# Performance work log

Hardware: AMD Instinct MI355X
Metric: run time of the kernel (lower is better)

## Reference

```python
import jax, jax.numpy as jnp
import numpy as np

B, S, D = 4, 2048, 1024
CTX_LEN, CTX_DIM = 77, 768
H, DH = 16, 64
INNER = H * DH
MULT = 4
EPS = 1e-5


def setup_inputs() -> dict:
    key = jax.random.key(0)
    ks = jax.random.split(key, 14)
    nrm = lambda k, shape: jax.random.normal(k, shape, dtype=jnp.float32) * 0.02
    return {
        "x": jax.random.normal(ks[0], (B, S, D), dtype=jnp.float32),
        "context": jax.random.normal(ks[1], (B, CTX_LEN, CTX_DIM), dtype=jnp.float32),
        "ln1_g": jnp.ones((D,), jnp.float32), "ln1_b": jnp.zeros((D,), jnp.float32),
        "ln2_g": jnp.ones((D,), jnp.float32), "ln2_b": jnp.zeros((D,), jnp.float32),
        "ln3_g": jnp.ones((D,), jnp.float32), "ln3_b": jnp.zeros((D,), jnp.float32),
        "a1_wq": nrm(ks[2], (D, INNER)), "a1_wk": nrm(ks[3], (D, INNER)),
        "a1_wv": nrm(ks[4], (D, INNER)), "a1_wo": nrm(ks[5], (INNER, D)),
        "a1_bo": jnp.zeros((D,), jnp.float32),
        "a2_wq": nrm(ks[6], (D, INNER)), "a2_wk": nrm(ks[7], (CTX_DIM, INNER)),
        "a2_wv": nrm(ks[8], (CTX_DIM, INNER)), "a2_wo": nrm(ks[9], (INNER, D)),
        "a2_bo": jnp.zeros((D,), jnp.float32),
        "ff_w1": nrm(ks[10], (D, D * MULT * 2)), "ff_b1": jnp.zeros((D * MULT * 2,), jnp.float32),
        "ff_w2": nrm(ks[11], (D * MULT, D)), "ff_b2": jnp.zeros((D,), jnp.float32),
    }


def _layernorm(x, g, b):
    mu = jnp.mean(x, axis=-1, keepdims=True)
    var = jnp.var(x, axis=-1, keepdims=True)
    return (x - mu) * jax.lax.rsqrt(var + EPS) * g + b


def _attn(xq, xkv, wq, wk, wv, wo, bo):
    b, sq, _ = xq.shape
    sk = xkv.shape[1]
    q = (xq @ wq).reshape(b, sq, H, DH)
    k = (xkv @ wk).reshape(b, sk, H, DH)
    v = (xkv @ wv).reshape(b, sk, H, DH)
    score = jnp.einsum('bqhd,bkhd->bhqk', q, k) * (DH ** -0.5)
    w = jax.nn.softmax(score, axis=-1)
    o = jnp.einsum('bhqk,bkhd->bqhd', w, v).reshape(b, sq, INNER)
    return o @ wo + bo


def _block(x, context, ln1_g, ln1_b, ln2_g, ln2_b, ln3_g, ln3_b,
           a1_wq, a1_wk, a1_wv, a1_wo, a1_bo,
           a2_wq, a2_wk, a2_wv, a2_wo, a2_bo,
           ff_w1, ff_b1, ff_w2, ff_b2):
    # self-attention
    x = _attn(_layernorm(x, ln1_g, ln1_b), _layernorm(x, ln1_g, ln1_b),
              a1_wq, a1_wk, a1_wv, a1_wo, a1_bo) + x
    # cross-attention
    x = _attn(_layernorm(x, ln2_g, ln2_b), context,
              a2_wq, a2_wk, a2_wv, a2_wo, a2_bo) + x
    # GeGLU feed-forward
    h = _layernorm(x, ln3_g, ln3_b) @ ff_w1 + ff_b1
    u, gate = jnp.split(h, 2, axis=-1)
    x = (u * jax.nn.gelu(gate, approximate=False)) @ ff_w2 + ff_b2 + x
    return x


def reference(x, context, ln1_g, ln1_b, ln2_g, ln2_b, ln3_g, ln3_b,
              a1_wq, a1_wk, a1_wv, a1_wo, a1_bo,
              a2_wq, a2_wk, a2_wv, a2_wo, a2_bo,
              ff_w1, ff_b1, ff_w2, ff_b2):
    return _block(x, context, ln1_g, ln1_b, ln2_g, ln2_b, ln3_g, ln3_b,
                  a1_wq, a1_wk, a1_wv, a1_wo, a1_bo,
                  a2_wq, a2_wk, a2_wv, a2_wo, a2_bo,
                  ff_w1, ff_b1, ff_w2, ff_b2)
```

## Files before the change

### kernel.cpp

```cpp
#include <hip/hip_runtime.h>
#include <hip/hip_bf16.h>
#include <math.h>

typedef __bf16 bf16;
typedef __bf16 bf16x8 __attribute__((ext_vector_type(8)));
typedef float f32x4 __attribute__((ext_vector_type(4)));

#define MFMA(a, b, c) __builtin_amdgcn_mfma_f32_16x16x32_bf16((a), (b), (c), 0, 0, 0)

static __device__ __forceinline__ void gl16(const bf16* g, bf16* l) {
  __builtin_amdgcn_global_load_lds(
      (const __attribute__((address_space(1))) void*)g,
      (__attribute__((address_space(3))) void*)l, 16, 0, 0);
}

static __device__ __forceinline__ bf16x8 bzero8() {
  bf16x8 v;
#pragma unroll
  for (int i = 0; i < 8; ++i) v[i] = (bf16)0.0f;
  return v;
}

__global__ void k_transpose_cvt(const float* __restrict__ W, bf16* __restrict__ Wt,
                                int K, int N) {
  __shared__ float tile[32][33];
  int k0 = blockIdx.x * 32, n0 = blockIdx.y * 32;
  int tx = threadIdx.x & 31, ty = threadIdx.x >> 5;
  for (int i = ty; i < 32; i += 8)
    tile[i][tx] = W[(size_t)(k0 + i) * N + (n0 + tx)];
  __syncthreads();
  for (int i = ty; i < 32; i += 8)
    Wt[(size_t)(n0 + i) * K + (k0 + tx)] = (bf16)tile[tx][i];
}

__global__ void k_transpose_v(const bf16* __restrict__ V, bf16* __restrict__ Vt,
                              int rows, int kvpad) {
  __shared__ __attribute__((aligned(16))) bf16 tile[64][72];
  int t0 = blockIdx.x * 64, h = blockIdx.y, b = blockIdx.z;
  int t = threadIdx.x;
  int tr = t >> 2, c0 = (t & 3) * 16;
  int token = t0 + tr;
  bf16x8 a = bzero8(), bv = bzero8();
  if (token < rows) {
    const bf16* src = V + ((size_t)(b * rows + token)) * 1024 + h * 64 + c0;
    a = *(const bf16x8*)src;
    bv = *(const bf16x8*)(src + 8);
  }
  *(bf16x8*)&tile[tr][c0] = a;
  *(bf16x8*)&tile[tr][c0 + 8] = bv;
  __syncthreads();
  int d = t >> 2, tq = (t & 3) * 16;
  bf16x8 o1, o2;
#pragma unroll
  for (int i = 0; i < 8; ++i) { o1[i] = tile[tq + i][d]; o2[i] = tile[tq + 8 + i][d]; }
  bf16* dst = Vt + ((size_t)((b * 16 + h) * 64 + d)) * kvpad + t0 + tq;
  *(bf16x8*)dst = o1;
  *(bf16x8*)(dst + 8) = o2;
}

__global__ void k_cvt(const float* __restrict__ in, bf16* __restrict__ out, int n) {
  int i = blockIdx.x * 256 + threadIdx.x;
  if (i < n) out[i] = (bf16)in[i];
}

__global__ void k_layernorm(const float* __restrict__ x, const float* __restrict__ g,
                            const float* __restrict__ b, bf16* __restrict__ out) {
  int row = blockIdx.x;
  float4 v = ((const float4*)(x + (size_t)row * 1024))[threadIdx.x];
  float s = v.x + v.y + v.z + v.w;
  float ss = v.x * v.x + v.y * v.y + v.z * v.z + v.w * v.w;
#pragma unroll
  for (int off = 1; off < 64; off <<= 1) {
    s += __shfl_xor(s, off);
    ss += __shfl_xor(ss, off);
  }
  __shared__ float sm[4], sm2[4];
  int w = threadIdx.x >> 6;
  if ((threadIdx.x & 63) == 0) { sm[w] = s; sm2[w] = ss; }
  __syncthreads();
  s = sm[0] + sm[1] + sm[2] + sm[3];
  ss = sm2[0] + sm2[1] + sm2[2] + sm2[3];
  float mu = s * (1.0f / 1024.0f);
  float var = ss * (1.0f / 1024.0f) - mu * mu;
  float rs = rsqrtf(var + 1e-5f);
  float4 gg = ((const float4*)g)[threadIdx.x];
  float4 bb = ((const float4*)b)[threadIdx.x];
  bf16* o = out + (size_t)row * 1024 + threadIdx.x * 4;
  o[0] = (bf16)((v.x - mu) * rs * gg.x + bb.x);
  o[1] = (bf16)((v.y - mu) * rs * gg.y + bb.y);
  o[2] = (bf16)((v.z - mu) * rs * gg.z + bb.z);
  o[3] = (bf16)((v.w - mu) * rs * gg.w + bb.w);
}

template <int EPI>
__global__ __launch_bounds__(256, 2)
void k_gemm_bt(const bf16* __restrict__ A, const bf16* __restrict__ Bt,
               const float* __restrict__ bias, const float* __restrict__ res,
               void* __restrict__ Cp, int M, int N, int K) {
  __shared__ __attribute__((aligned(16))) bf16 As[128 * 32];
  __shared__ __attribute__((aligned(16))) bf16 Bs[128 * 32];
  int m0 = blockIdx.x * 128, n0 = blockIdx.y * 128;
  int tid = threadIdx.x, lane = tid & 63, wave = tid >> 6;
  int wm = (wave >> 1) * 64, wn = (wave & 1) * 64;
  int quad = lane >> 4, l15 = lane & 15;
  f32x4 acc[4][4];
#pragma unroll
  for (int i = 0; i < 4; ++i)
#pragma unroll
    for (int j = 0; j < 4; ++j)
#pragma unroll
      for (int r = 0; r < 4; ++r) acc[i][j][r] = 0.0f;
  int srow = wave * 16 + (lane >> 2), scol = (lane & 3) * 8;
  const bf16* ga = A + (size_t)(m0 + srow) * K + scol;
  const bf16* gb = Bt + (size_t)(n0 + srow) * K + scol;
  bf16* la = As + srow * 32 + scol;
  bf16* lb = Bs + srow * 32 + scol;
  for (int k0 = 0; k0 < K; k0 += 32) {
    gl16(ga, la);
    gl16(ga + (size_t)64 * K, la + 64 * 32);
    gl16(gb, lb);
    gl16(gb + (size_t)64 * K, lb + 64 * 32);
    ga += 32; gb += 32;
    __syncthreads();
    bf16x8 af[4], bfr[4];
#pragma unroll
    for (int i = 0; i < 4; ++i) af[i] = *(const bf16x8*)(&As[(wm + i * 16 + l15) * 32 + quad * 8]);
#pragma unroll
    for (int i = 0; i < 4; ++i) bfr[i] = *(const bf16x8*)(&Bs[(wn + i * 16 + l15) * 32 + quad * 8]);
#pragma unroll
    for (int mi = 0; mi < 4; ++mi)
#pragma unroll
      for (int ni = 0; ni < 4; ++ni)
        acc[mi][ni] = MFMA(af[mi], bfr[ni], acc[mi][ni]);
    __syncthreads();
  }
#pragma unroll
  for (int mi = 0; mi < 4; ++mi) {
#pragma unroll
    for (int r = 0; r < 4; ++r) {
      int row = m0 + wm + mi * 16 + quad * 4 + r;
      if (row >= M) continue;
#pragma unroll
      for (int ni = 0; ni < 4; ++ni) {
        int col = n0 + wn + ni * 16 + l15;
        float v = acc[mi][ni][r];
        if (EPI == 0) {
          ((bf16*)Cp)[(size_t)row * N + col] = (bf16)v;
        } else {
          ((float*)Cp)[(size_t)row * N + col] =
              v + bias[col] + res[(size_t)row * N + col];
        }
      }
    }
  }
}

__global__ __launch_bounds__(256, 2)
void k_gemm_geglu(const bf16* __restrict__ A, const bf16* __restrict__ W1t,
                  const float* __restrict__ b1, bf16* __restrict__ Hg,
                  int M, int K) {
  __shared__ __attribute__((aligned(16))) bf16 As[128 * 32];
  __shared__ __attribute__((aligned(16))) bf16 Bu[128 * 32];
  __shared__ __attribute__((aligned(16))) bf16 Bg[128 * 32];
  const int N = 4096;
  int m0 = blockIdx.x * 128, n0 = blockIdx.y * 128;
  int tid = threadIdx.x, lane = tid & 63, wave = tid >> 6;
  int wm = (wave >> 1) * 64, wn = (wave & 1) * 64;
  int quad = lane >> 4, l15 = lane & 15;
  f32x4 accu[4][4], accg[4][4];
#pragma unroll
  for (int i = 0; i < 4; ++i)
#pragma unroll
    for (int j = 0; j < 4; ++j)
#pragma unroll
      for (int r = 0; r < 4; ++r) { accu[i][j][r] = 0.0f; accg[i][j][r] = 0.0f; }
  int srow = wave * 16 + (lane >> 2), scol = (lane & 3) * 8;
  const bf16* ga = A + (size_t)(m0 + srow) * K + scol;
  const bf16* gu = W1t + (size_t)(n0 + srow) * K + scol;
  const bf16* gg = W1t + (size_t)(n0 + srow + 4096) * K + scol;
  bf16* la = As + srow * 32 + scol;
  bf16* lu = Bu + srow * 32 + scol;
  bf16* lg = Bg + srow * 32 + scol;
  for (int k0 = 0; k0 < K; k0 += 32) {
    gl16(ga, la);
    gl16(ga + (size_t)64 * K, la + 64 * 32);
    gl16(gu, lu);
    gl16(gu + (size_t)64 * K, lu + 64 * 32);
    gl16(gg, lg);
    gl16(gg + (size_t)64 * K, lg + 64 * 32);
    ga += 32; gu += 32; gg += 32;
    __syncthreads();
    bf16x8 af[4], bu[4], bg[4];
#pragma unroll
    for (int i = 0; i < 4; ++i) af[i] = *(const bf16x8*)(&As[(wm + i * 16 + l15) * 32 + quad * 8]);
#pragma unroll
    for (int i = 0; i < 4; ++i) bu[i] = *(const bf16x8*)(&Bu[(wn + i * 16 + l15) * 32 + quad * 8]);
#pragma unroll
    for (int i = 0; i < 4; ++i) bg[i] = *(const bf16x8*)(&Bg[(wn + i * 16 + l15) * 32 + quad * 8]);
#pragma unroll
    for (int mi = 0; mi < 4; ++mi)
#pragma unroll
      for (int ni = 0; ni < 4; ++ni) {
        accu[mi][ni] = MFMA(af[mi], bu[ni], accu[mi][ni]);
        accg[mi][ni] = MFMA(af[mi], bg[ni], accg[mi][ni]);
      }
    __syncthreads();
  }
#pragma unroll
  for (int mi = 0; mi < 4; ++mi)
#pragma unroll
    for (int r = 0; r < 4; ++r) {
      int row = m0 + wm + mi * 16 + quad * 4 + r;
#pragma unroll
      for (int ni = 0; ni < 4; ++ni) {
        int col = n0 + wn + ni * 16 + l15;
        float u = accu[mi][ni][r] + b1[col];
        float g = accg[mi][ni][r] + b1[col + 4096];
        float ge = 0.5f * g * (1.0f + erff(g * 0.70710678118654752f));
        Hg[(size_t)row * N + col] = (bf16)(u * ge);
      }
    }
}

#define CSC 0.18033688011112042f
__global__ __launch_bounds__(256, 4)
void k_flash(const bf16* __restrict__ Q, const bf16* __restrict__ Kb,
             const bf16* __restrict__ VtG, bf16* __restrict__ O,
             int Sq, int Sk, int kvrows, int kvpad) {
  __shared__ __attribute__((aligned(16))) bf16 Ks[2][64 * 64];
  __shared__ __attribute__((aligned(16))) bf16 Vs[2][64 * 64];
  __shared__ __attribute__((aligned(16))) bf16 Ps[4][16 * 64];
  int qt = blockIdx.x, h = blockIdx.y, b = blockIdx.z;
  int tid = threadIdx.x, lane = tid & 63, wave = tid >> 6;
  int quad = lane >> 4, l15 = lane & 15;
  const bf16* qsrc = Q + (size_t)(b * Sq + qt * 64 + wave * 16 + l15) * 1024 + h * 64 + quad * 8;
  bf16x8 aq0 = *(const bf16x8*)qsrc;
  bf16x8 aq1 = *(const bf16x8*)(qsrc + 32);
  bf16x8 ones8;
#pragma unroll
  for (int i = 0; i < 8; ++i) ones8[i] = (bf16)1.0f;

  float m_r[4], l_r[4];
  f32x4 acc_o[4];
#pragma unroll
  for (int r = 0; r < 4; ++r) { m_r[r] = -1e30f; l_r[r] = 0.0f; }
#pragma unroll
  for (int ni = 0; ni < 4; ++ni)
#pragma unroll
    for (int r = 0; r < 4; ++r) acc_o[ni][r] = 0.0f;

  int srow = tid >> 3;
  int scol = ((tid & 7) * 8) ^ ((srow & 7) << 3);
  const bf16* kg0 = Kb + (size_t)(b * kvrows + srow) * 1024 + h * 64 + scol;
  const bf16* vg0 = VtG + ((size_t)((b * 16 + h) * 64 + srow)) * kvpad + scol;

  int nt = (Sk + 63) >> 6;
  {
    gl16(kg0, &Ks[0][tid * 8]);
    gl16(kg0 + (size_t)32 * 1024, &Ks[0][2048 + tid * 8]);
    gl16(vg0, &Vs[0][tid * 8]);
    gl16(vg0 + (size_t)32 * kvpad, &Vs[0][2048 + tid * 8]);
  }
  __syncthreads();

  int cur = 0;
  for (int t = 0; t < nt; ++t) {
    int k0 = t << 6;
    if (t + 1 < nt) {
      const bf16* kg = kg0 + (size_t)(k0 + 64) * 1024;
      const bf16* vg = vg0 + (k0 + 64);
      gl16(kg, &Ks[cur ^ 1][tid * 8]);
      gl16(kg + (size_t)32 * 1024, &Ks[cur ^ 1][2048 + tid * 8]);
      gl16(vg, &Vs[cur ^ 1][tid * 8]);
      gl16(vg + (size_t)32 * kvpad, &Vs[cur ^ 1][2048 + tid * 8]);
    }
    const bf16* Kc = &Ks[cur][0];
    const bf16* Vc = &Vs[cur][0];

    f32x4 sacc[4];
#pragma unroll
    for (int ni = 0; ni < 4; ++ni)
#pragma unroll
      for (int r = 0; r < 4; ++r) sacc[ni][r] = 0.0f;
#pragma unroll
    for (int ni = 0; ni < 4; ++ni) {
      int krow = ni * 16 + l15;
      int sw = (krow & 7) << 3;
      bf16x8 bk0 = *(const bf16x8*)&Kc[krow * 64 + ((quad * 8) ^ sw)];
      bf16x8 bk1 = *(const bf16x8*)&Kc[krow * 64 + ((32 + quad * 8) ^ sw)];
      sacc[ni] = MFMA(aq0, bk0, sacc[ni]);
      sacc[ni] = MFMA(aq1, bk1, sacc[ni]);
    }
    if (k0 + 64 > Sk) {
#pragma unroll
      for (int ni = 0; ni < 4; ++ni) {
        bool oob = (k0 + ni * 16 + l15 >= Sk);
#pragma unroll
        for (int r = 0; r < 4; ++r)
          if (oob) sacc[ni][r] = -1e30f;
      }
    }
    float alpha[4], mC[4];
#pragma unroll
    for (int r = 0; r < 4; ++r) {
      float v = fmaxf(fmaxf(sacc[0][r], sacc[1][r]), fmaxf(sacc[2][r], sacc[3][r]));
#pragma unroll
      for (int off = 1; off < 16; off <<= 1) v = fmaxf(v, __shfl_xor(v, off));
      float mn = fmaxf(m_r[r], v);
      alpha[r] = __builtin_amdgcn_exp2f((m_r[r] - mn) * CSC);
      m_r[r] = mn;
      mC[r] = mn * CSC;
    }
    bf16* ps = &Ps[wave][0];
#pragma unroll
    for (int ni = 0; ni < 4; ++ni) {
      int col = ni * 16 + l15;
#pragma unroll
      for (int r = 0; r < 4; ++r) {
        int prow = quad * 4 + r;
        ps[prow * 64 + (col ^ ((prow & 7) << 3))] =
            (bf16)__builtin_amdgcn_exp2f(sacc[ni][r] * CSC - mC[r]);
      }
    }
    int swp = (l15 & 7) << 3;
    bf16x8 ap0 = *(const bf16x8*)&ps[l15 * 64 + ((quad * 8) ^ swp)];
    bf16x8 ap1 = *(const bf16x8*)&ps[l15 * 64 + ((32 + quad * 8) ^ swp)];
    f32x4 psum;
#pragma unroll
    for (int r = 0; r < 4; ++r) psum[r] = 0.0f;
    psum = MFMA(ap0, ones8, psum);
    psum = MFMA(ap1, ones8, psum);
#pragma unroll
    for (int r = 0; r < 4; ++r) l_r[r] = l_r[r] * alpha[r] + psum[r];
#pragma unroll
    for (int ni = 0; ni < 4; ++ni) {
#pragma unroll
      for (int r = 0; r < 4; ++r) acc_o[ni][r] *= alpha[r];
      int vrow = ni * 16 + l15;
      int sw = (vrow & 7) << 3;
      bf16x8 bv0 = *(const bf16x8*)&Vc[vrow * 64 + ((quad * 8) ^ sw)];
      bf16x8 bv1 = *(const bf16x8*)&Vc[vrow * 64 + ((32 + quad * 8) ^ sw)];
      acc_o[ni] = MFMA(ap0, bv0, acc_o[ni]);
      acc_o[ni] = MFMA(ap1, bv1, acc_o[ni]);
    }
    __syncthreads();
    cur ^= 1;
  }
#pragma unroll
  for (int ni = 0; ni < 4; ++ni)
#pragma unroll
    for (int r = 0; r < 4; ++r) {
      int q = qt * 64 + wave * 16 + quad * 4 + r;
      float ov = acc_o[ni][r] / l_r[r];
      O[(size_t)(b * Sq + q) * 1024 + h * 64 + ni * 16 + l15] = (bf16)ov;
    }
}

extern "C" void kernel_launch(void* const* d_in, const int* in_sizes, int n_in,
                              void* d_out, int out_size, void* d_ws, size_t ws_size,
                              hipStream_t stream) {
  (void)in_sizes; (void)n_in; (void)out_size; (void)ws_size;
  const float* x = (const float*)d_in[0];
  const float* ctx = (const float*)d_in[1];
  const float* ln1_g = (const float*)d_in[2];
  const float* ln1_b = (const float*)d_in[3];
  const float* ln2_g = (const float*)d_in[4];
  const float* ln2_b = (const float*)d_in[5];
  const float* ln3_g = (const float*)d_in[6];
  const float* ln3_b = (const float*)d_in[7];
  const float* a1_wq = (const float*)d_in[8];
  const float* a1_wk = (const float*)d_in[9];
  const float* a1_wv = (const float*)d_in[10];
  const float* a1_wo = (const float*)d_in[11];
  const float* a1_bo = (const float*)d_in[12];
  const float* a2_wq = (const float*)d_in[13];
  const float* a2_wk = (const float*)d_in[14];
  const float* a2_wv = (const float*)d_in[15];
  const float* a2_wo = (const float*)d_in[16];
  const float* a2_bo = (const float*)d_in[17];
  const float* ff_w1 = (const float*)d_in[18];
  const float* ff_b1 = (const float*)d_in[19];
  const float* ff_w2 = (const float*)d_in[20];
  const float* ff_b2 = (const float*)d_in[21];
  float* xout = (float*)d_out;

  const int M = 4 * 2048;
  char* ws = (char*)d_ws;
  size_t off = 0;
  auto alloc = [&](size_t elems) -> bf16* {
    bf16* p = (bf16*)(ws + off);
    off += ((elems * sizeof(bf16)) + 255) & ~(size_t)255;
    return p;
  };
  bf16* wq1t = alloc((size_t)1024 * 1024);
  bf16* wk1t = alloc((size_t)1024 * 1024);
  bf16* wv1t = alloc((size_t)1024 * 1024);
  bf16* wo1t = alloc((size_t)1024 * 1024);
  bf16* wq2t = alloc((size_t)1024 * 1024);
  bf16* wk2t = alloc((size_t)1024 * 768);
  bf16* wv2t = alloc((size_t)1024 * 768);
  bf16* wo2t = alloc((size_t)1024 * 1024);
  bf16* w1t = alloc((size_t)8192 * 1024);
  bf16* w2t = alloc((size_t)1024 * 4096);
  bf16* lnb = alloc((size_t)M * 1024);
  bf16* qb = alloc((size_t)M * 1024);
  bf16* kb = alloc((size_t)M * 1024);
  bf16* vb = alloc((size_t)M * 1024);
  bf16* ab = alloc((size_t)M * 1024);
  bf16* ctxb = alloc((size_t)308 * 768);
  bf16* kcb = alloc((size_t)308 * 1024);
  bf16* vcb = alloc((size_t)308 * 1024);
  bf16* hgb = alloc((size_t)M * 4096);
  bf16* vtb = hgb;
  bf16* vtcb = hgb + (size_t)4 * 16 * 64 * 2048;

  hipMemcpyAsync(xout, x, (size_t)M * 1024 * sizeof(float),
                 hipMemcpyDeviceToDevice, stream);

  k_transpose_cvt<<<dim3(32, 32), 256, 0, stream>>>(a1_wq, wq1t, 1024, 1024);
  k_transpose_cvt<<<dim3(32, 32), 256, 0, stream>>>(a1_wk, wk1t, 1024, 1024);
  k_transpose_cvt<<<dim3(32, 32), 256, 0, stream>>>(a1_wv, wv1t, 1024, 1024);
  k_transpose_cvt<<<dim3(32, 32), 256, 0, stream>>>(a1_wo, wo1t, 1024, 1024);
  k_transpose_cvt<<<dim3(32, 32), 256, 0, stream>>>(a2_wq, wq2t, 1024, 1024);
  k_transpose_cvt<<<dim3(24, 32), 256, 0, stream>>>(a2_wk, wk2t, 768, 1024);
  k_transpose_cvt<<<dim3(24, 32), 256, 0, stream>>>(a2_wv, wv2t, 768, 1024);
  k_transpose_cvt<<<dim3(32, 32), 256, 0, stream>>>(a2_wo, wo2t, 1024, 1024);
  k_transpose_cvt<<<dim3(32, 256), 256, 0, stream>>>(ff_w1, w1t, 1024, 8192);
  k_transpose_cvt<<<dim3(128, 32), 256, 0, stream>>>(ff_w2, w2t, 4096, 1024);
  k_cvt<<<(308 * 768 + 255) / 256, 256, 0, stream>>>(ctx, ctxb, 308 * 768);

  k_layernorm<<<M, 256, 0, stream>>>(xout, ln1_g, ln1_b, lnb);
  k_gemm_bt<0><<<dim3(64, 8), 256, 0, stream>>>(lnb, wq1t, nullptr, nullptr, qb, M, 1024, 1024);
  k_gemm_bt<0><<<dim3(64, 8), 256, 0, stream>>>(lnb, wk1t, nullptr, nullptr, kb, M, 1024, 1024);
  k_gemm_bt<0><<<dim3(64, 8), 256, 0, stream>>>(lnb, wv1t, nullptr, nullptr, vb, M, 1024, 1024);
  k_transpose_v<<<dim3(32, 16, 4), 256, 0, stream>>>(vb, vtb, 2048, 2048);
  k_flash<<<dim3(32, 16, 4), 256, 0, stream>>>(qb, kb, vtb, ab, 2048, 2048, 2048, 2048);
  k_gemm_bt<1><<<dim3(64, 8), 256, 0, stream>>>(ab, wo1t, a1_bo, xout, xout, M, 1024, 1024);

  k_layernorm<<<M, 256, 0, stream>>>(xout, ln2_g, ln2_b, lnb);
  k_gemm_bt<0><<<dim3(64, 8), 256, 0, stream>>>(lnb, wq2t, nullptr, nullptr, qb, M, 1024, 1024);
  k_gemm_bt<0><<<dim3(3, 8), 256, 0, stream>>>(ctxb, wk2t, nullptr, nullptr, kcb, 308, 1024, 768);
  k_gemm_bt<0><<<dim3(3, 8), 256, 0, stream>>>(ctxb, wv2t, nullptr, nullptr, vcb, 308, 1024, 768);
  k_transpose_v<<<dim3(2, 16, 4), 256, 0, stream>>>(vcb, vtcb, 77, 128);
  k_flash<<<dim3(32, 16, 4), 256, 0, stream>>>(qb, kcb, vtcb, ab, 2048, 77, 77, 128);
  k_gemm_bt<1><<<dim3(64, 8), 256, 0, stream>>>(ab, wo2t, a2_bo, xout, xout, M, 1024, 1024);

  k_layernorm<<<M, 256, 0, stream>>>(xout, ln3_g, ln3_b, lnb);
  k_gemm_geglu<<<dim3(64, 32), 256, 0, stream>>>(lnb, w1t, ff_b1, hgb, M, 1024);
  k_gemm_bt<1><<<dim3(64, 8), 256, 0, stream>>>(hgb, w2t, ff_b2, xout, xout, M, 1024, 4096);
}
```

Baseline: 901.4 us.

## Double-buffer GeGLU GEMM LDS tiles and XOR-swizzle shared layout

Splits the A, up and gate LDS tiles into two buffers so the async global-to-LDS loads for the next K step are issued before computing the current one, removing one barrier per iteration. The LDS layout is also XOR-swizzled on the 8-element column group by row, to reduce bank conflicts on fragment reads. This doubles LDS usage per block, which may limit occupancy.

```diff
diff --git a/kernel.cpp b/kernel.cpp
--- a/kernel.cpp
+++ b/kernel.cpp
@@ -159,9 +159,9 @@
 void k_gemm_geglu(const bf16* __restrict__ A, const bf16* __restrict__ W1t,
                   const float* __restrict__ b1, bf16* __restrict__ Hg,
                   int M, int K) {
-  __shared__ __attribute__((aligned(16))) bf16 As[128 * 32];
-  __shared__ __attribute__((aligned(16))) bf16 Bu[128 * 32];
-  __shared__ __attribute__((aligned(16))) bf16 Bg[128 * 32];
+  __shared__ __attribute__((aligned(16))) bf16 As[2][128 * 32];
+  __shared__ __attribute__((aligned(16))) bf16 Bu[2][128 * 32];
+  __shared__ __attribute__((aligned(16))) bf16 Bg[2][128 * 32];
   const int N = 4096;
   int m0 = blockIdx.x * 128, n0 = blockIdx.y * 128;
   int tid = threadIdx.x, lane = tid & 63, wave = tid >> 6;
@@ -174,29 +174,36 @@
     for (int j = 0; j < 4; ++j)
 #pragma unroll
       for (int r = 0; r < 4; ++r) { accu[i][j][r] = 0.0f; accg[i][j][r] = 0.0f; }
-  int srow = wave * 16 + (lane >> 2), scol = (lane & 3) * 8;
+  int srow = tid >> 2;
+  int scol = ((tid & 3) * 8) ^ ((srow & 3) << 3);
+  int ldst = tid * 8;
   const bf16* ga = A + (size_t)(m0 + srow) * K + scol;
   const bf16* gu = W1t + (size_t)(n0 + srow) * K + scol;
   const bf16* gg = W1t + (size_t)(n0 + srow + 4096) * K + scol;
-  bf16* la = As + srow * 32 + scol;
-  bf16* lu = Bu + srow * 32 + scol;
-  bf16* lg = Bg + srow * 32 + scol;
+  auto stage = [&](int buf, int k0) {
+    gl16(ga + k0, &As[buf][ldst]);
+    gl16(ga + k0 + (size_t)64 * K, &As[buf][2048 + ldst]);
+    gl16(gu + k0, &Bu[buf][ldst]);
+    gl16(gu + k0 + (size_t)64 * K, &Bu[buf][2048 + ldst]);
+    gl16(gg + k0, &Bg[buf][ldst]);
+    gl16(gg + k0 + (size_t)64 * K, &Bg[buf][2048 + ldst]);
+  };
+  stage(0, 0);
+  __syncthreads();
+  int asw = (l15 & 3) << 3;
+  int cur = 0;
   for (int k0 = 0; k0 < K; k0 += 32) {
-    gl16(ga, la);
-    gl16(ga + (size_t)64 * K, la + 64 * 32);
-    gl16(gu, lu);
-    gl16(gu + (size_t)64 * K, lu + 64 * 32);
-    gl16(gg, lg);
-    gl16(gg + (size_t)64 * K, lg + 64 * 32);
-    ga += 32; gu += 32; gg += 32;
-    __syncthreads();
+    if (k0 + 32 < K) stage(cur ^ 1, k0 + 32);
     bf16x8 af[4], bu[4], bg[4];
 #pragma unroll
-    for (int i = 0; i < 4; ++i) af[i] = *(const bf16x8*)(&As[(wm + i * 16 + l15) * 32 + quad * 8]);
-#pragma unroll
-    for (int i = 0; i < 4; ++i) bu[i] = *(const bf16x8*)(&Bu[(wn + i * 16 + l15) * 32 + quad * 8]);
-#pragma unroll
-    for (int i = 0; i < 4; ++i) bg[i] = *(const bf16x8*)(&Bg[(wn + i * 16 + l15) * 32 + quad * 8]);
+    for (int i = 0; i < 4; ++i)
+      af[i] = *(const bf16x8*)(&As[cur][(wm + i * 16 + l15) * 32 + ((quad * 8) ^ asw)]);
+#pragma unroll
+    for (int i = 0; i < 4; ++i)
+      bu[i] = *(const bf16x8*)(&Bu[cur][(wn + i * 16 + l15) * 32 + ((quad * 8) ^ asw)]);
+#pragma unroll
+    for (int i = 0; i < 4; ++i)
+      bg[i] = *(const bf16x8*)(&Bg[cur][(wn + i * 16 + l15) * 32 + ((quad * 8) ^ asw)]);
 #pragma unroll
     for (int mi = 0; mi < 4; ++mi)
 #pragma unroll
@@ -205,6 +212,7 @@
         accg[mi][ni] = MFMA(af[mi], bg[ni], accg[mi][ni]);
       }
     __syncthreads();
+    cur ^= 1;
   }
 #pragma unroll
   for (int mi = 0; mi < 4; ++mi)
```

Measured after the change: 910.1 us. About the same (+1.0%).

## Triple-buffer LDS tiles in GEMM kernels with async global-to-LDS prefetch

Applied to the files above, without the earlier changes.

Both the generic bt-GEMM and the fused GeGLU GEMM now use a 3-stage LDS ring. They issue global_load_lds for the tile two steps ahead while MFMAs run on the current tile, and synchronize with explicit vmcnt waits plus a single barrier per iteration instead of two __syncthreads. The aim is to hide global-load latency behind compute that previously stalled on each tile. The cost is 3x the LDS per block, which may reduce occupancy, especially for the GeGLU kernel (72KB), and launch_bounds is raised to 3 for the generic GEMM.

```diff
diff --git a/kernel.cpp b/kernel.cpp
--- a/kernel.cpp
+++ b/kernel.cpp
@@ -93,12 +93,12 @@
 }
 
 template <int EPI>
-__global__ __launch_bounds__(256, 2)
+__global__ __launch_bounds__(256, 3)
 void k_gemm_bt(const bf16* __restrict__ A, const bf16* __restrict__ Bt,
                const float* __restrict__ bias, const float* __restrict__ res,
                void* __restrict__ Cp, int M, int N, int K) {
-  __shared__ __attribute__((aligned(16))) bf16 As[128 * 32];
-  __shared__ __attribute__((aligned(16))) bf16 Bs[128 * 32];
+  __shared__ __attribute__((aligned(16))) bf16 As[3][128 * 32];
+  __shared__ __attribute__((aligned(16))) bf16 Bs[3][128 * 32];
   int m0 = blockIdx.x * 128, n0 = blockIdx.y * 128;
   int tid = threadIdx.x, lane = tid & 63, wave = tid >> 6;
   int wm = (wave >> 1) * 64, wn = (wave & 1) * 64;
@@ -113,26 +113,47 @@
   int srow = wave * 16 + (lane >> 2), scol = (lane & 3) * 8;
   const bf16* ga = A + (size_t)(m0 + srow) * K + scol;
   const bf16* gb = Bt + (size_t)(n0 + srow) * K + scol;
-  bf16* la = As + srow * 32 + scol;
-  bf16* lb = Bs + srow * 32 + scol;
-  for (int k0 = 0; k0 < K; k0 += 32) {
-    gl16(ga, la);
-    gl16(ga + (size_t)64 * K, la + 64 * 32);
-    gl16(gb, lb);
-    gl16(gb + (size_t)64 * K, lb + 64 * 32);
-    ga += 32; gb += 32;
-    __syncthreads();
+  int lofs = srow * 32 + scol;
+  auto stage = [&](int buf, int k0) {
+    gl16(ga + k0, &As[buf][lofs]);
+    gl16(ga + k0 + (size_t)64 * K, &As[buf][64 * 32 + lofs]);
+    gl16(gb + k0, &Bs[buf][lofs]);
+    gl16(gb + k0 + (size_t)64 * K, &Bs[buf][64 * 32 + lofs]);
+  };
+  int nt = K >> 5;
+  stage(0, 0);
+  if (nt > 1) {
+    stage(1, 32);
+    asm volatile("s_waitcnt vmcnt(4)" ::: "memory");
+  } else {
+    asm volatile("s_waitcnt vmcnt(0)" ::: "memory");
+  }
+  __builtin_amdgcn_s_barrier();
+  int cb = 0;
+  for (int t = 0; t < nt; ++t) {
+    int pb = cb + 2; if (pb >= 3) pb -= 3;
+    if (t + 2 < nt) stage(pb, (t + 2) << 5);
+    const bf16* Ac = &As[cb][0];
+    const bf16* Bc = &Bs[cb][0];
     bf16x8 af[4], bfr[4];
 #pragma unroll
-    for (int i = 0; i < 4; ++i) af[i] = *(const bf16x8*)(&As[(wm + i * 16 + l15) * 32 + quad * 8]);
-#pragma unroll
-    for (int i = 0; i < 4; ++i) bfr[i] = *(const bf16x8*)(&Bs[(wn + i * 16 + l15) * 32 + quad * 8]);
+    for (int i = 0; i < 4; ++i) af[i] = *(const bf16x8*)(&Ac[(wm + i * 16 + l15) * 32 + quad * 8]);
+#pragma unroll
+    for (int i = 0; i < 4; ++i) bfr[i] = *(const bf16x8*)(&Bc[(wn + i * 16 + l15) * 32 + quad * 8]);
 #pragma unroll
     for (int mi = 0; mi < 4; ++mi)
 #pragma unroll
       for (int ni = 0; ni < 4; ++ni)
         acc[mi][ni] = MFMA(af[mi], bfr[ni], acc[mi][ni]);
-    __syncthreads();
+    __builtin_amdgcn_sched_barrier(0);
+    if (t + 2 < nt) {
+      asm volatile("s_waitcnt vmcnt(4)" ::: "memory");
+      __builtin_amdgcn_s_barrier();
+    } else if (t + 1 < nt) {
+      asm volatile("s_waitcnt vmcnt(0)" ::: "memory");
+      __builtin_amdgcn_s_barrier();
+    }
+    if (++cb == 3) cb = 0;
   }
 #pragma unroll
   for (int mi = 0; mi < 4; ++mi) {
@@ -159,9 +180,9 @@
 void k_gemm_geglu(const bf16* __restrict__ A, const bf16* __restrict__ W1t,
                   const float* __restrict__ b1, bf16* __restrict__ Hg,
                   int M, int K) {
-  __shared__ __attribute__((aligned(16))) bf16 As[128 * 32];
-  __shared__ __attribute__((aligned(16))) bf16 Bu[128 * 32];
-  __shared__ __attribute__((aligned(16))) bf16 Bg[128 * 32];
+  __shared__ __attribute__((aligned(16))) bf16 As[3][128 * 32];
+  __shared__ __attribute__((aligned(16))) bf16 Bu[3][128 * 32];
+  __shared__ __attribute__((aligned(16))) bf16 Bg[3][128 * 32];
   const int N = 4096;
   int m0 = blockIdx.x * 128, n0 = blockIdx.y * 128;
   int tid = threadIdx.x, lane = tid & 63, wave = tid >> 6;
@@ -178,25 +199,38 @@
   const bf16* ga = A + (size_t)(m0 + srow) * K + scol;
   const bf16* gu = W1t + (size_t)(n0 + srow) * K + scol;
   const bf16* gg = W1t + (size_t)(n0 + srow + 4096) * K + scol;
-  bf16* la = As + srow * 32 + scol;
-  bf16* lu = Bu + srow * 32 + scol;
-  bf16* lg = Bg + srow * 32 + scol;
-  for (int k0 = 0; k0 < K; k0 += 32) {
-    gl16(ga, la);
-    gl16(ga + (size_t)64 * K, la + 64 * 32);
-    gl16(gu, lu);
-    gl16(gu + (size_t)64 * K, lu + 64 * 32);
-    gl16(gg, lg);
-    gl16(gg + (size_t)64 * K, lg + 64 * 32);
-    ga += 32; gu += 32; gg += 32;
-    __syncthreads();
+  int lofs = srow * 32 + scol;
+  auto stage = [&](int buf, int k0) {
+    gl16(ga + k0, &As[buf][lofs]);
+    gl16(ga + k0 + (size_t)64 * K, &As[buf][64 * 32 + lofs]);
+    gl16(gu + k0, &Bu[buf][lofs]);
+    gl16(gu + k0 + (size_t)64 * K, &Bu[buf][64 * 32 + lofs]);
+    gl16(gg + k0, &Bg[buf][lofs]);
+    gl16(gg + k0 + (size_t)64 * K, &Bg[buf][64 * 32 + lofs]);
+  };
+  int nt = K >> 5;
+  stage(0, 0);
+  if (nt > 1) {
+    stage(1, 32);
+    asm volatile("s_waitcnt vmcnt(6)" ::: "memory");
+  } else {
+    asm volatile("s_waitcnt vmcnt(0)" ::: "memory");
+  }
+  __builtin_amdgcn_s_barrier();
+  int cb = 0;
+  for (int t = 0; t < nt; ++t) {
+    int pb = cb + 2; if (pb >= 3) pb -= 3;
+    if (t + 2 < nt) stage(pb, (t + 2) << 5);
+    const bf16* Ac = &As[cb][0];
+    const bf16* Uc = &Bu[cb][0];
+    const bf16* Gc = &Bg[cb][0];
     bf16x8 af[4], bu[4], bg[4];
 #pragma unroll
-    for (int i = 0; i < 4; ++i) af[i] = *(const bf16x8*)(&As[(wm + i * 16 + l15) * 32 + quad * 8]);
-#pragma unroll
-    for (int i = 0; i < 4; ++i) bu[i] = *(const bf16x8*)(&Bu[(wn + i * 16 + l15) * 32 + quad * 8]);
-#pragma unroll
-    for (int i = 0; i < 4; ++i) bg[i] = *(const bf16x8*)(&Bg[(wn + i * 16 + l15) * 32 + quad * 8]);
+    for (int i = 0; i < 4; ++i) af[i] = *(const bf16x8*)(&Ac[(wm + i * 16 + l15) * 32 + quad * 8]);
+#pragma unroll
+    for (int i = 0; i < 4; ++i) bu[i] = *(const bf16x8*)(&Uc[(wn + i * 16 + l15) * 32 + quad * 8]);
+#pragma unroll
+    for (int i = 0; i < 4; ++i) bg[i] = *(const bf16x8*)(&Gc[(wn + i * 16 + l15) * 32 + quad * 8]);
 #pragma unroll
     for (int mi = 0; mi < 4; ++mi)
 #pragma unroll
@@ -204,7 +238,15 @@
         accu[mi][ni] = MFMA(af[mi], bu[ni], accu[mi][ni]);
         accg[mi][ni] = MFMA(af[mi], bg[ni], accg[mi][ni]);
       }
-    __syncthreads();
+    __builtin_amdgcn_sched_barrier(0);
+    if (t + 2 < nt) {
+      asm volatile("s_waitcnt vmcnt(6)" ::: "memory");
+      __builtin_amdgcn_s_barrier();
+    } else if (t + 1 < nt) {
+      asm volatile("s_waitcnt vmcnt(0)" ::: "memory");
+      __builtin_amdgcn_s_barrier();
+    }
+    if (++cb == 3) cb = 0;
   }
 #pragma unroll
   for (int mi = 0; mi < 4; ++mi)
```

After: 910.7 us. No clear change (+1.0%).

## Add pipelined 256x256 GEMM kernel for fused QKV and GeGLU projections

Applied to the files above, without the earlier changes.

Introduces a 512-thread GEMM with 256x256 tiles, 64-wide K steps, double-buffered async global-to-LDS loads with XOR swizzle and manual waitcnt/barrier pipelining. The three self-attention Q/K/V projections are merged into one launch over a concatenated transposed weight. The GeGLU weight is permuted at transpose time so each tile holds matching u and gate columns, with the gelu product formed through LDS in the epilogue. The aim is higher MFMA utilisation and fewer launches, at the cost of more register pressure and fragile hand-tuned synchronisation.

```diff
diff --git a/kernel.cpp b/kernel.cpp
--- a/kernel.cpp
+++ b/kernel.cpp
@@ -21,13 +21,15 @@
   return v;
 }
 
+template <int PERM>
 __global__ void k_transpose_cvt(const float* __restrict__ W, bf16* __restrict__ Wt,
                                 int K, int N) {
   __shared__ float tile[32][33];
   int k0 = blockIdx.x * 32, n0 = blockIdx.y * 32;
+  int src_n0 = PERM ? (((n0 >> 8) << 7) + (n0 & 127) + (((n0 >> 7) & 1) << 12)) : n0;
   int tx = threadIdx.x & 31, ty = threadIdx.x >> 5;
   for (int i = ty; i < 32; i += 8)
-    tile[i][tx] = W[(size_t)(k0 + i) * N + (n0 + tx)];
+    tile[i][tx] = W[(size_t)(k0 + i) * N + (src_n0 + tx)];
   __syncthreads();
   for (int i = ty; i < 32; i += 8)
     Wt[(size_t)(n0 + i) * K + (k0 + tx)] = (bf16)tile[tx][i];
@@ -155,71 +157,148 @@
   }
 }
 
-__global__ __launch_bounds__(256, 2)
-void k_gemm_geglu(const bf16* __restrict__ A, const bf16* __restrict__ W1t,
-                  const float* __restrict__ b1, bf16* __restrict__ Hg,
-                  int M, int K) {
-  __shared__ __attribute__((aligned(16))) bf16 As[128 * 32];
-  __shared__ __attribute__((aligned(16))) bf16 Bu[128 * 32];
-  __shared__ __attribute__((aligned(16))) bf16 Bg[128 * 32];
-  const int N = 4096;
-  int m0 = blockIdx.x * 128, n0 = blockIdx.y * 128;
+template <int EPI>
+__global__ __launch_bounds__(512, 2)
+void k_gemm256(const bf16* __restrict__ A, const bf16* __restrict__ Bt,
+               const float* __restrict__ b1, void* __restrict__ Cp,
+               int M, int K) {
+  __shared__ __attribute__((aligned(16))) bf16 As[2][2][128 * 64];
+  __shared__ __attribute__((aligned(16))) bf16 Bs[2][2][128 * 64];
+  int m0 = blockIdx.x * 256, n0 = blockIdx.y * 256;
   int tid = threadIdx.x, lane = tid & 63, wave = tid >> 6;
-  int wm = (wave >> 1) * 64, wn = (wave & 1) * 64;
+  int wr = wave >> 2, wc = wave & 3;
   int quad = lane >> 4, l15 = lane & 15;
-  f32x4 accu[4][4], accg[4][4];
-#pragma unroll
-  for (int i = 0; i < 4; ++i)
+  int rsw = (l15 & 4) << 2;
+  f32x4 acc[8][4];
+#pragma unroll
+  for (int i = 0; i < 8; ++i)
 #pragma unroll
     for (int j = 0; j < 4; ++j)
 #pragma unroll
-      for (int r = 0; r < 4; ++r) { accu[i][j][r] = 0.0f; accg[i][j][r] = 0.0f; }
-  int srow = wave * 16 + (lane >> 2), scol = (lane & 3) * 8;
-  const bf16* ga = A + (size_t)(m0 + srow) * K + scol;
-  const bf16* gu = W1t + (size_t)(n0 + srow) * K + scol;
-  const bf16* gg = W1t + (size_t)(n0 + srow + 4096) * K + scol;
-  bf16* la = As + srow * 32 + scol;
-  bf16* lu = Bu + srow * 32 + scol;
-  bf16* lg = Bg + srow * 32 + scol;
-  for (int k0 = 0; k0 < K; k0 += 32) {
-    gl16(ga, la);
-    gl16(ga + (size_t)64 * K, la + 64 * 32);
-    gl16(gu, lu);
-    gl16(gu + (size_t)64 * K, lu + 64 * 32);
-    gl16(gg, lg);
-    gl16(gg + (size_t)64 * K, lg + 64 * 32);
-    ga += 32; gu += 32; gg += 32;
+      for (int r = 0; r < 4; ++r) acc[i][j][r] = 0.0f;
+  int srow = tid >> 3;
+  int scol = ((tid & 7) * 8) ^ ((srow & 4) << 2);
+  int t8 = tid * 8;
+  const bf16* gA = A + (size_t)(m0 + srow) * K + scol;
+  const bf16* gB = Bt + (size_t)(n0 + srow) * K + scol;
+  const int NT = K >> 6;
+  auto stageHalf = [&](int h) {
+    int tile = h >> 2, c = h & 3, slot = tile & 1;
+    int k0 = tile << 6;
+    if (c < 2) {
+      const bf16* s = gB + (size_t)(c * 128) * K + k0;
+      gl16(s, &Bs[slot][c][t8]);
+      gl16(s + (size_t)64 * K, &Bs[slot][c][4096 + t8]);
+    } else {
+      const bf16* s = gA + (size_t)((c - 2) * 128) * K + k0;
+      gl16(s, &As[slot][c - 2][t8]);
+      gl16(s + (size_t)64 * K, &As[slot][c - 2][4096 + t8]);
+    }
+  };
+#pragma unroll
+  for (int h = 0; h < 7; ++h) stageHalf(h);
+  asm volatile("s_waitcnt vmcnt(6)" ::: "memory");
+  asm volatile("s_barrier" ::: "memory");
+
+  bf16x8 bfr[4][2];
+  int NTh = NT >> 1;
+  for (int t = 0; t < NTh; ++t) {
+#pragma unroll
+    for (int q8 = 0; q8 < 8; ++q8) {
+      const int slot = q8 >> 2, q = q8 & 3;
+      const bf16* Ah = &As[slot][wr][0];
+      const bf16* Bh = &Bs[slot][wc >> 1][0];
+      bf16x8 afr[2][2];
+#pragma unroll
+      for (int m2 = 0; m2 < 2; ++m2)
+#pragma unroll
+        for (int kk = 0; kk < 2; ++kk)
+          afr[m2][kk] = *(const bf16x8*)&Ah[((q * 2 + m2) * 16 + l15) * 64 +
+                                            ((kk * 32 + quad * 8) ^ rsw)];
+      if (q == 0) {
+#pragma unroll
+        for (int ni = 0; ni < 4; ++ni)
+#pragma unroll
+          for (int kk = 0; kk < 2; ++kk)
+            bfr[ni][kk] = *(const bf16x8*)&Bh[((wc & 1) * 64 + ni * 16 + l15) * 64 +
+                                              ((kk * 32 + quad * 8) ^ rsw)];
+      }
+      int H = t * 8 + q8 + 7;
+      if (H < 4 * NT) stageHalf(H);
+      asm volatile("s_barrier" ::: "memory");
+      asm volatile("s_waitcnt lgkmcnt(0)" ::: "memory");
+      __builtin_amdgcn_sched_barrier(0);
+      __builtin_amdgcn_s_setprio(1);
+#pragma unroll
+      for (int m2 = 0; m2 < 2; ++m2)
+#pragma unroll
+        for (int ni = 0; ni < 4; ++ni) {
+          acc[q * 2 + m2][ni] = MFMA(afr[m2][0], bfr[ni][0], acc[q * 2 + m2][ni]);
+          acc[q * 2 + m2][ni] = MFMA(afr[m2][1], bfr[ni][1], acc[q * 2 + m2][ni]);
+        }
+      __builtin_amdgcn_s_setprio(0);
+      if (q == 3) {
+        if (t * 8 + q8 == 4 * NT - 5)
+          asm volatile("s_waitcnt vmcnt(0)" ::: "memory");
+        else
+          asm volatile("s_waitcnt vmcnt(6)" ::: "memory");
+      }
+      asm volatile("s_barrier" ::: "memory");
+    }
+  }
+  if (EPI == 0) {
+    int seg = n0 >> 10;
+    int cl0 = (n0 & 1023) + wc * 64;
+    bf16* outp = (bf16*)Cp + (size_t)seg * M * 1024;
+#pragma unroll
+    for (int mi = 0; mi < 8; ++mi)
+#pragma unroll
+      for (int r = 0; r < 4; ++r) {
+        int row = m0 + wr * 128 + mi * 16 + quad * 4 + r;
+#pragma unroll
+        for (int ni = 0; ni < 4; ++ni)
+          outp[(size_t)row * 1024 + cl0 + ni * 16 + l15] = (bf16)acc[mi][ni][r];
+      }
+  } else {
+    bf16* Xg = &As[0][0][0];
+    int cb = blockIdx.y * 128;
+    if (wc >= 2) {
+      int gc0 = (wc - 2) * 64;
+#pragma unroll
+      for (int mi = 0; mi < 8; ++mi)
+#pragma unroll
+        for (int ni = 0; ni < 4; ++ni) {
+          int col = gc0 + ni * 16 + l15;
+          float bg = b1[4096 + cb + col];
+#pragma unroll
+          for (int r = 0; r < 4; ++r) {
+            int rowl = wr * 128 + mi * 16 + quad * 4 + r;
+            float g = acc[mi][ni][r] + bg;
+            float ge = 0.5f * g * (1.0f + erff(g * 0.70710678118654752f));
+            Xg[rowl * 128 + col] = (bf16)ge;
+          }
+        }
+    }
     __syncthreads();
-    bf16x8 af[4], bu[4], bg[4];
-#pragma unroll
-    for (int i = 0; i < 4; ++i) af[i] = *(const bf16x8*)(&As[(wm + i * 16 + l15) * 32 + quad * 8]);
-#pragma unroll
-    for (int i = 0; i < 4; ++i) bu[i] = *(const bf16x8*)(&Bu[(wn + i * 16 + l15) * 32 + quad * 8]);
-#pragma unroll
-    for (int i = 0; i < 4; ++i) bg[i] = *(const bf16x8*)(&Bg[(wn + i * 16 + l15) * 32 + quad * 8]);
-#pragma unroll
-    for (int mi = 0; mi < 4; ++mi)
-#pragma unroll
-      for (int ni = 0; ni < 4; ++ni) {
-        accu[mi][ni] = MFMA(af[mi], bu[ni], accu[mi][ni]);
-        accg[mi][ni] = MFMA(af[mi], bg[ni], accg[mi][ni]);
-      }
-    __syncthreads();
-  }
-#pragma unroll
-  for (int mi = 0; mi < 4; ++mi)
-#pragma unroll
-    for (int r = 0; r < 4; ++r) {
-      int row = m0 + wm + mi * 16 + quad * 4 + r;
-#pragma unroll
-      for (int ni = 0; ni < 4; ++ni) {
-        int col = n0 + wn + ni * 16 + l15;
-        float u = accu[mi][ni][r] + b1[col];
-        float g = accg[mi][ni][r] + b1[col + 4096];
-        float ge = 0.5f * g * (1.0f + erff(g * 0.70710678118654752f));
-        Hg[(size_t)row * N + col] = (bf16)(u * ge);
-      }
-    }
+    if (wc < 2) {
+      int uc0 = wc * 64;
+      bf16* Hg = (bf16*)Cp;
+#pragma unroll
+      for (int mi = 0; mi < 8; ++mi)
+#pragma unroll
+        for (int ni = 0; ni < 4; ++ni) {
+          int col = uc0 + ni * 16 + l15;
+          float bu = b1[cb + col];
+#pragma unroll
+          for (int r = 0; r < 4; ++r) {
+            int rowl = wr * 128 + mi * 16 + quad * 4 + r;
+            float u = acc[mi][ni][r] + bu;
+            float hv = u * (float)Xg[rowl * 128 + col];
+            Hg[(size_t)(m0 + rowl) * 4096 + cb + col] = (bf16)hv;
+          }
+        }
+    }
+  }
 }
 
 #define CSC 0.18033688011112042f
@@ -392,9 +471,7 @@
     off += ((elems * sizeof(bf16)) + 255) & ~(size_t)255;
     return p;
   };
-  bf16* wq1t = alloc((size_t)1024 * 1024);
-  bf16* wk1t = alloc((size_t)1024 * 1024);
-  bf16* wv1t = alloc((size_t)1024 * 1024);
+  bf16* wqkv1t = alloc((size_t)3072 * 1024);
   bf16* wo1t = alloc((size_t)1024 * 1024);
   bf16* wq2t = alloc((size_t)1024 * 1024);
   bf16* wk2t = alloc((size_t)1024 * 768);
@@ -417,22 +494,20 @@
   hipMemcpyAsync(xout, x, (size_t)M * 1024 * sizeof(float),
                  hipMemcpyDeviceToDevice, stream);
 
-  k_transpose_cvt<<<dim3(32, 32), 256, 0, stream>>>(a1_wq, wq1t, 1024, 1024);
-  k_transpose_cvt<<<dim3(32, 32), 256, 0, stream>>>(a1_wk, wk1t, 1024, 1024);
-  k_transpose_cvt<<<dim3(32, 32), 256, 0, stream>>>(a1_wv, wv1t, 1024, 1024);
-  k_transpose_cvt<<<dim3(32, 32), 256, 0, stream>>>(a1_wo, wo1t, 1024, 1024);
-  k_transpose_cvt<<<dim3(32, 32), 256, 0, stream>>>(a2_wq, wq2t, 1024, 1024);
-  k_transpose_cvt<<<dim3(24, 32), 256, 0, stream>>>(a2_wk, wk2t, 768, 1024);
-  k_transpose_cvt<<<dim3(24, 32), 256, 0, stream>>>(a2_wv, wv2t, 768, 1024);
-  k_transpose_cvt<<<dim3(32, 32), 256, 0, stream>>>(a2_wo, wo2t, 1024, 1024);
-  k_transpose_cvt<<<dim3(32, 256), 256, 0, stream>>>(ff_w1, w1t, 1024, 8192);
-  k_transpose_cvt<<<dim3(128, 32), 256, 0, stream>>>(ff_w2, w2t, 4096, 1024);
+  k_transpose_cvt<0><<<dim3(32, 32), 256, 0, stream>>>(a1_wq, wqkv1t, 1024, 1024);
+  k_transpose_cvt<0><<<dim3(32, 32), 256, 0, stream>>>(a1_wk, wqkv1t + (size_t)1024 * 1024, 1024, 1024);
+  k_transpose_cvt<0><<<dim3(32, 32), 256, 0, stream>>>(a1_wv, wqkv1t + (size_t)2048 * 1024, 1024, 1024);
+  k_transpose_cvt<0><<<dim3(32, 32), 256, 0, stream>>>(a1_wo, wo1t, 1024, 1024);
+  k_transpose_cvt<0><<<dim3(32, 32), 256, 0, stream>>>(a2_wq, wq2t, 1024, 1024);
+  k_transpose_cvt<0><<<dim3(24, 32), 256, 0, stream>>>(a2_wk, wk2t, 768, 1024);
+  k_transpose_cvt<0><<<dim3(24, 32), 256, 0, stream>>>(a2_wv, wv2t, 768, 1024);
+  k_transpose_cvt<0><<<dim3(32, 32), 256, 0, stream>>>(a2_wo, wo2t, 1024, 1024);
+  k_transpose_cvt<1><<<dim3(32, 256), 256, 0, stream>>>(ff_w1, w1t, 1024, 8192);
+  k_transpose_cvt<0><<<dim3(128, 32), 256, 0, stream>>>(ff_w2, w2t, 4096, 1024);
   k_cvt<<<(308 * 768 + 255) / 256, 256, 0, stream>>>(ctx, ctxb, 308 * 768);
 
   k_layernorm<<<M, 256, 0, stream>>>(xout, ln1_g, ln1_b, lnb);
-  k_gemm_bt<0><<<dim3(64, 8), 256, 0, stream>>>(lnb, wq1t, nullptr, nullptr, qb, M, 1024, 1024);
-  k_gemm_bt<0><<<dim3(64, 8), 256, 0, stream>>>(lnb, wk1t, nullptr, nullptr, kb, M, 1024, 1024);
-  k_gemm_bt<0><<<dim3(64, 8), 256, 0, stream>>>(lnb, wv1t, nullptr, nullptr, vb, M, 1024, 1024);
+  k_gemm256<0><<<dim3(32, 12), 512, 0, stream>>>(lnb, wqkv1t, nullptr, qb, M, 1024);
   k_transpose_v<<<dim3(32, 16, 4), 256, 0, stream>>>(vb, vtb, 2048, 2048);
   k_flash<<<dim3(32, 16, 4), 256, 0, stream>>>(qb, kb, vtb, ab, 2048, 2048, 2048, 2048);
   k_gemm_bt<1><<<dim3(64, 8), 256, 0, stream>>>(ab, wo1t, a1_bo, xout, xout, M, 1024, 1024);
@@ -446,6 +521,6 @@
   k_gemm_bt<1><<<dim3(64, 8), 256, 0, stream>>>(ab, wo2t, a2_bo, xout, xout, M, 1024, 1024);
 
   k_layernorm<<<M, 256, 0, stream>>>(xout, ln3_g, ln3_b, lnb);
-  k_gemm_geglu<<<dim3(64, 32), 256, 0, stream>>>(lnb, w1t, ff_b1, hgb, M, 1024);
+  k_gemm256<1><<<dim3(32, 32), 512, 0, stream>>>(lnb, w1t, ff_b1, hgb, M, 1024);
   k_gemm_bt<1><<<dim3(64, 8), 256, 0, stream>>>(hgb, w2t, ff_b2, xout, xout, M, 1024, 4096);
 }
```

After: 926.0 us. 2.7% more time.
